# Kernel optimization log

Hardware: AMD Instinct MI355X
Metric: run time of the kernel (lower is better)

The kernel has to match this reference:

```python
import jax, jax.numpy as jnp
import numpy as np

POOLING_COUNTS = [15, 8, 8]
N_CLIPS = 64


def build_mask_and_indices(pooling_counts, N):
    """Replicates the static index construction in __init__ (pure numpy)."""
    mask2d = np.zeros((N, N), dtype=bool)
    mask2d[np.arange(N), np.arange(N)] = True
    maskij = []
    pool_specs = []  # (kernel, stride) for each level
    for gi, c in enumerate(pooling_counts):
        if gi == 0:
            pool_specs.extend([(2, 1)] * c)
        else:
            pool_specs.extend([(3, 2)] + [(2, 1)] * (c - 1))
    stride, offset = 1, 0
    for c in pooling_counts:
        for _ in range(c):
            offset += stride
            i = np.arange(0, N - offset, stride)
            j = np.arange(offset, N, stride)
            mask2d[i, j] = True
            maskij.append((i, j))
        stride *= 2
    return mask2d, maskij, pool_specs


def maxpool1d(x, k, s):
    # x: [B, D, L]; MaxPool1d(kernel=k, stride=s), no padding
    L = x.shape[-1]
    out_len = (L - k) // s + 1
    idx = np.arange(out_len)[:, None] * s + np.arange(k)[None, :]  # [out_len, k]
    return x[..., idx].max(axis=-1)


def setup_inputs() -> dict:
    key = jax.random.key(0)
    x = jax.random.normal(key, (16, 512, N_CLIPS), dtype=jnp.float32)
    return {"x": x}


def reference(x):
    B, D, N = x.shape
    mask2d_np, maskij, pool_specs = build_mask_and_indices(POOLING_COUNTS, N)
    diag = np.arange(N)

    # diagonal scatter: map2d[:, :, n, n] = x[:, :, n]
    base = jnp.zeros((B, D, N, N), dtype=x.dtype).at[:, :, diag, diag].set(x)

    # boundary map: average of endpoint features at each (i, j) line
    boundary_map2d = base
    for i, j in maskij:
        boundary_map2d = boundary_map2d.at[:, :, i, j].set((x[:, :, i] + x[:, :, j]) * 0.5)

    # content map: pyramid of max-pools scattered onto the same lines
    content_map2d = base
    xp = x
    for (k, s), (i, j) in zip(pool_specs, maskij):
        xp = maxpool1d(xp, k, s)
        content_map2d = content_map2d.at[:, :, i, j].set(xp)

    mask2d = jnp.broadcast_to(jnp.asarray(mask2d_np)[None, None], (B, 1, N, N))
    return boundary_map2d, content_map2d, mask2d
```

## Files before the change

### kernel.cpp

```cpp
#include <hip/hip_runtime.h>


__device__ __forceinline__ bool on_line(int i, int off) {
    return (off <= 15)
        || ((off & 1) && off >= 17 && off <= 31 && !(i & 1))
        || (((off & 3) == 3) && off >= 35 && !(i & 3));
}

__global__ __launch_bounds__(256) void sbc_kernel(const float* __restrict__ x,
                                                  float* __restrict__ out,
                                                  size_t mapsz) {
    __shared__ float sp[7][64];
    const int bd = blockIdx.x;
    const int t  = threadIdx.x;

    if (t < 64) sp[0][t] = x[(size_t)bd * 64 + t];
    __syncthreads();
#pragma unroll
    for (int k = 1; k < 7; ++k) {
        if (t < 64) {
            const int w = 1 << (k - 1);
            float v = sp[k - 1][t];
            if (t + w < 64) v = fmaxf(v, sp[k - 1][t + w]);
            sp[k][t] = v;
        }
        __syncthreads();
    }

    const size_t bbase = (size_t)bd * 4096;
#pragma unroll
    for (int it = 0; it < 4; ++it) {
        const int p4 = t + it * 256;
        const int p  = p4 << 2;
        const int i  = p >> 6;
        const int j0 = p & 63;
        const float xi = sp[0][i];
        float bb[4], cc[4];
#pragma unroll
        for (int q = 0; q < 4; ++q) {
            const int j = j0 + q;
            float b = 0.0f, c = 0.0f;
            if (j == i) {
                b = xi; c = xi;
            } else if (j > i) {
                const int off = j - i;
                if (on_line(i, off)) {
                    b = 0.5f * (xi + sp[0][j]);
                    const int k = 31 - __clz(off + 1);
                    c = fmaxf(sp[k][i], sp[k][j + 1 - (1 << k)]);
                }
            }
            bb[q] = b; cc[q] = c;
        }
        *(float4*)(out + bbase + p)         = make_float4(bb[0], bb[1], bb[2], bb[3]);
        *(float4*)(out + mapsz + bbase + p) = make_float4(cc[0], cc[1], cc[2], cc[3]);
    }

    if ((bd & 511) == 0) {
        const int b = bd >> 9;
        float* mout = out + 2 * mapsz + (size_t)b * 4096;
#pragma unroll
        for (int it = 0; it < 4; ++it) {
            const int p4 = t + it * 256;
            const int p  = p4 << 2;
            const int i  = p >> 6;
            const int j0 = p & 63;
            float mm[4];
#pragma unroll
            for (int q = 0; q < 4; ++q) {
                const int j = j0 + q;
                bool on = (j == i) || (j > i && on_line(i, j - i));
                mm[q] = on ? 1.0f : 0.0f;
            }
            *(float4*)(mout + p) = make_float4(mm[0], mm[1], mm[2], mm[3]);
        }
    }
}

extern "C" void kernel_launch(void* const* d_in, const int* in_sizes, int n_in,
                              void* d_out, int out_size, void* d_ws, size_t ws_size,
                              hipStream_t stream) {
    const float* x = (const float*)d_in[0];
    float* out = (float*)d_out;
    const int N  = 64;
    const int BD = in_sizes[0] / N;
    const size_t mapsz = (size_t)BD * N * N;
    sbc_kernel<<<dim3(BD), dim3(256), 0, stream>>>(x, out, mapsz);
}
```

Before: 259.2 us.

## Rewrite as wave-per-tile kernel using lane shuffles and precomputed column bitmask

Replaces the shared-memory max-pool pyramid and block-per-tile layout with one 64-lane wave handling two (b,d) tiles. Each lane owns column j, broadcasts x[i] with shuffles, keeps a running max for the content map, and uses a per-column 64-bit mask to decide which entries are on the line. This removes shared memory and barriers, but writes are now scalar float stores per row instead of float4 stores, and there are 64 shuffles per tile.

```diff
diff --git a/kernel.cpp b/kernel.cpp
--- a/kernel.cpp
+++ b/kernel.cpp
@@ -1,78 +1,52 @@
 #include <hip/hip_runtime.h>
 
 
-__device__ __forceinline__ bool on_line(int i, int off) {
-    return (off <= 15)
-        || ((off & 1) && off >= 17 && off <= 31 && !(i & 1))
-        || (((off & 3) == 3) && off >= 35 && !(i & 3));
-}
+#define T_PER_WAVE 2
 
 __global__ __launch_bounds__(256) void sbc_kernel(const float* __restrict__ x,
                                                   float* __restrict__ out,
                                                   size_t mapsz) {
-    __shared__ float sp[7][64];
-    const int bd = blockIdx.x;
-    const int t  = threadIdx.x;
+    const int lane = threadIdx.x & 63;
+    const int wid  = blockIdx.x * 4 + (threadIdx.x >> 6);
+    const int j    = lane;
 
-    if (t < 64) sp[0][t] = x[(size_t)bd * 64 + t];
-    __syncthreads();
+    const int sh = 63 - j;
+    const unsigned long long mbits =
+          (1ULL << j)
+        | (0x7FFF000000000000ULL >> sh)
+        | ((0x0000555500000000ULL >> sh) & 0x5555555555555555ULL)
+        | ((0x0000000011111111ULL >> sh) & 0x1111111111111111ULL);
+
+    const int tile0 = wid * T_PER_WAVE;
+
+    float xv[T_PER_WAVE];
 #pragma unroll
-    for (int k = 1; k < 7; ++k) {
-        if (t < 64) {
-            const int w = 1 << (k - 1);
-            float v = sp[k - 1][t];
-            if (t + w < 64) v = fmaxf(v, sp[k - 1][t + w]);
-            sp[k][t] = v;
+    for (int tt = 0; tt < T_PER_WAVE; ++tt)
+        xv[tt] = x[(size_t)(tile0 + tt) * 64 + j];
+
+#pragma unroll
+    for (int tt = 0; tt < T_PER_WAVE; ++tt) {
+        const int tile = tile0 + tt;
+        float* __restrict__ bout = out + (size_t)tile * 4096;
+        float* __restrict__ cout = bout + mapsz;
+        const float xj = xv[tt];
+        float r = xj;
+#pragma unroll
+        for (int i = 63; i >= 0; --i) {
+            const float xi = __shfl(xv[tt], i, 64);
+            const float xs = (j >= i) ? xi : -INFINITY;
+            r = fmaxf(r, xs);
+            const bool on  = (mbits >> i) & 1ULL;
+            const float s  = on ? 0.5f : 0.0f;
+            const float s2 = on ? 1.0f : 0.0f;
+            bout[i * 64 + j] = s * (xi + xj);
+            cout[i * 64 + j] = s2 * r;
         }
-        __syncthreads();
-    }
-
-    const size_t bbase = (size_t)bd * 4096;
+        if ((tile & 511) == 0) {
+            float* __restrict__ mout = out + 2 * mapsz + (size_t)(tile >> 9) * 4096;
 #pragma unroll
-    for (int it = 0; it < 4; ++it) {
-        const int p4 = t + it * 256;
-        const int p  = p4 << 2;
-        const int i  = p >> 6;
-        const int j0 = p & 63;
-        const float xi = sp[0][i];
-        float bb[4], cc[4];
-#pragma unroll
-        for (int q = 0; q < 4; ++q) {
-            const int j = j0 + q;
-            float b = 0.0f, c = 0.0f;
-            if (j == i) {
-                b = xi; c = xi;
-            } else if (j > i) {
-                const int off = j - i;
-                if (on_line(i, off)) {
-                    b = 0.5f * (xi + sp[0][j]);
-                    const int k = 31 - __clz(off + 1);
-                    c = fmaxf(sp[k][i], sp[k][j + 1 - (1 << k)]);
-                }
-            }
-            bb[q] = b; cc[q] = c;
-        }
-        *(float4*)(out + bbase + p)         = make_float4(bb[0], bb[1], bb[2], bb[3]);
-        *(float4*)(out + mapsz + bbase + p) = make_float4(cc[0], cc[1], cc[2], cc[3]);
-    }
-
-    if ((bd & 511) == 0) {
-        const int b = bd >> 9;
-        float* mout = out + 2 * mapsz + (size_t)b * 4096;
-#pragma unroll
-        for (int it = 0; it < 4; ++it) {
-            const int p4 = t + it * 256;
-            const int p  = p4 << 2;
-            const int i  = p >> 6;
-            const int j0 = p & 63;
-            float mm[4];
-#pragma unroll
-            for (int q = 0; q < 4; ++q) {
-                const int j = j0 + q;
-                bool on = (j == i) || (j > i && on_line(i, j - i));
-                mm[q] = on ? 1.0f : 0.0f;
-            }
-            *(float4*)(mout + p) = make_float4(mm[0], mm[1], mm[2], mm[3]);
+            for (int i = 0; i < 64; ++i)
+                mout[i * 64 + j] = ((mbits >> i) & 1ULL) ? 1.0f : 0.0f;
         }
     }
 }
@@ -85,5 +59,6 @@
     const int N  = 64;
     const int BD = in_sizes[0] / N;
     const size_t mapsz = (size_t)BD * N * N;
-    sbc_kernel<<<dim3(BD), dim3(256), 0, stream>>>(x, out, mapsz);
+    const int nwaves = BD / T_PER_WAVE;
+    sbc_kernel<<<dim3(nwaves / 4), dim3(256), 0, stream>>>(x, out, mapsz);
 }
```

New measurement: 250.3 us, median of 2. 1.04x faster.
